# Performance work log

Hardware: AMD Instinct MI355X
Metric: run time of the kernel (lower is better)

## Reference

```python
import jax, jax.numpy as jnp
import numpy as np

D = 1024
HS = 64
NH = D // HS
NEG_INF = -1e30


def setup_inputs() -> dict:
    key = jax.random.key(0)
    ks = jax.random.split(key, 8)
    B, S = 4, 2048
    x = jax.random.normal(ks[0], (B, S, D), dtype=jnp.float32)
    y = jax.random.normal(ks[1], (B, S, D), dtype=jnp.float32)
    pad_mask = jnp.ones((B, S), dtype=jnp.int32)
    time_attention = jnp.ones((S, S), dtype=jnp.int32)
    scale = 1.0 / np.sqrt(D)
    Wq = jax.random.normal(ks[2], (D, D), dtype=jnp.float32) * scale
    Wk = jax.random.normal(ks[3], (D, D), dtype=jnp.float32) * scale
    Wv = jax.random.normal(ks[4], (D, D), dtype=jnp.float32) * scale
    Wp = jax.random.normal(ks[5], (D, D), dtype=jnp.float32) * scale
    bp = jnp.zeros((D,), dtype=jnp.float32)
    return {"x": x, "y": y, "pad_mask": pad_mask, "time_attention": time_attention,
            "Wq": Wq, "Wk": Wk, "Wv": Wv, "Wp": Wp, "bp": bp}


def reference(x, y, pad_mask, time_attention, Wq, Wk, Wv, Wp, bp):
    B, S, _ = x.shape
    Sy = y.shape[1]
    # q/k/v projections (Linear: x @ W.T), split into heads -> [B, H, S, hs]
    q = (y @ Wq.T).reshape(B, Sy, NH, HS).transpose(0, 2, 1, 3)
    k = (x @ Wk.T).reshape(B, S, NH, HS).transpose(0, 2, 1, 3)
    v = (x @ Wv.T).reshape(B, S, NH, HS).transpose(0, 2, 1, 3)
    # scaled scores [B, H, Sy, S]
    att = jnp.einsum('bhqe,bhke->bhqk', q, k) * (HS ** -0.5)
    # causal mask (tril[:S, :S])
    causal = jnp.tril(jnp.ones((S, S), dtype=jnp.bool_))
    att = jnp.where(causal[None, None, :Sy, :], att, NEG_INF)
    # pad mask over kv positions
    att = jnp.where(pad_mask[:, None, None, :] != 0, att, NEG_INF)
    # time attention mask [Sq, Sk]
    att = jnp.where(time_attention[None, None, :Sy, :] != 0, att, NEG_INF)
    p = jax.nn.softmax(att, axis=-1)  # dropout p=0 -> identity
    out = jnp.einsum('bhqk,bhke->bhqe', p, v)
    out = out.transpose(0, 2, 1, 3).reshape(B, Sy, D)
    return out @ Wp.T + bp
```

## Files before the change

### kernel.cpp

```cpp
#include <hip/hip_runtime.h>
#include <hip/hip_bf16.h>
#include <stdint.h>
#include <stddef.h>


typedef __attribute__((ext_vector_type(4))) float f32x4;
typedef __attribute__((ext_vector_type(8))) short s16x8;
typedef __attribute__((ext_vector_type(4))) float float4v;
typedef __attribute__((ext_vector_type(2))) unsigned int u32x2;

#define DEV __device__ __forceinline__

constexpr int Bsz = 4, Sseq = 2048, Dm = 1024, NHn = 16, HSn = 64;
constexpr float QSCALE = 0.125f * 1.4426950408889634f;

constexpr size_t SZ_BF_XY = (size_t)Bsz * Sseq * Dm * 2;
constexpr size_t SZ_W     = (size_t)Dm * Dm * 2;
constexpr size_t OFF_XBF  = 0;
constexpr size_t OFF_YBF  = OFF_XBF + SZ_BF_XY;
constexpr size_t OFF_WQ   = OFF_YBF + SZ_BF_XY;
constexpr size_t OFF_WK   = OFF_WQ + SZ_W;
constexpr size_t OFF_WV   = OFF_WK + SZ_W;
constexpr size_t OFF_WP   = OFF_WV + SZ_W;
constexpr size_t OFF_QWS  = OFF_WP + SZ_W;
constexpr size_t OFF_KWS  = OFF_QWS + SZ_BF_XY;
constexpr size_t OFF_VTWS = OFF_KWS + SZ_BF_XY;
constexpr size_t OFF_OWS  = OFF_VTWS + SZ_BF_XY;
constexpr size_t OFF_FLAG = OFF_OWS + SZ_BF_XY;

DEV unsigned short f2bf(float f) {
  union { float f; unsigned int u; } v; v.f = f;
  unsigned int r = (v.u + 0x7FFFu + ((v.u >> 16) & 1u)) >> 16;
  return (unsigned short)r;
}

DEV void gll16(const void* g, void* l) {
  __builtin_amdgcn_global_load_lds((const __attribute__((address_space(1))) unsigned int*)g,
                                   (__attribute__((address_space(3))) unsigned int*)l, 16, 0, 0);
}

DEV unsigned int cvtpk(float a, float b) {
  unsigned int r;
  asm("v_cvt_pk_bf16_f32 %0, %1, %2" : "=v"(r) : "v"(a), "v"(b));
  return r;
}

__global__ void cvt_all(const float* __restrict__ x, const float* __restrict__ y,
                        const float* __restrict__ Wq, const float* __restrict__ Wk,
                        const float* __restrict__ Wv, const float* __restrict__ Wp,
                        char* __restrict__ ws) {
  const int blk = blockIdx.x;
  const float* src;
  unsigned short* dst;
  int b8;
  float scale = 1.f;
  if (blk < 4096)      { src = x;  dst = (unsigned short*)(ws + OFF_XBF); b8 = blk; }
  else if (blk < 8192) { src = y;  dst = (unsigned short*)(ws + OFF_YBF); b8 = blk - 4096; }
  else if (blk < 8704) { src = Wq; dst = (unsigned short*)(ws + OFF_WQ);  b8 = blk - 8192; scale = QSCALE; }
  else if (blk < 9216) { src = Wk; dst = (unsigned short*)(ws + OFF_WK);  b8 = blk - 8704; }
  else if (blk < 9728) { src = Wv; dst = (unsigned short*)(ws + OFF_WV);  b8 = blk - 9216; }
  else                 { src = Wp; dst = (unsigned short*)(ws + OFF_WP);  b8 = blk - 9728; }
  const size_t i = (size_t)b8 * 256 + threadIdx.x;
  const float4v* s = (const float4v*)src + i * 2;
  float4v a = s[0], b = s[1];
  s16x8 o;
  o[0] = (short)f2bf(a[0] * scale); o[1] = (short)f2bf(a[1] * scale);
  o[2] = (short)f2bf(a[2] * scale); o[3] = (short)f2bf(a[3] * scale);
  o[4] = (short)f2bf(b[0] * scale); o[5] = (short)f2bf(b[1] * scale);
  o[6] = (short)f2bf(b[2] * scale); o[7] = (short)f2bf(b[3] * scale);
  *(s16x8*)(dst + i * 8) = o;
}

__global__ void init_flag(int* f) { f[0] = 1; }
__global__ void check_mask(const int* __restrict__ p, int n, int* __restrict__ f) {
  int bad = 0;
  for (int i = blockIdx.x * blockDim.x + threadIdx.x; i < n; i += gridDim.x * blockDim.x)
    bad |= (p[i] == 0);
  if (bad) atomicAnd(f, 0);
}

DEV void gemm_core(const unsigned short* __restrict__ A, const unsigned short* __restrict__ W,
                   unsigned short* __restrict__ lA, unsigned short* __restrict__ lB,
                   f32x4 (&acc)[4][4], int m0, int n0, int w, int lane, int lo, int hi,
                   int wm, int wn) {
  constexpr int K = 1024;
  for (int k0 = 0; k0 < K; k0 += 32) {
#pragma unroll
    for (int h = 0; h < 2; ++h) {
      int c = w * 64 + h * 256 + lane;
      gll16(A + (size_t)(m0 + (c >> 2)) * K + k0 + (c & 3) * 8, lA + (size_t)(w * 64 + h * 256) * 8);
      gll16(W + (size_t)(n0 + (c >> 2)) * K + k0 + (c & 3) * 8, lB + (size_t)(w * 64 + h * 256) * 8);
    }
    __syncthreads();
    s16x8 af[4], bfr[4];
#pragma unroll
    for (int mi = 0; mi < 4; ++mi) af[mi] = *(const s16x8*)&lA[(wm * 64 + mi * 16 + lo) * 32 + hi * 8];
#pragma unroll
    for (int ni = 0; ni < 4; ++ni) bfr[ni] = *(const s16x8*)&lB[(wn * 64 + ni * 16 + lo) * 32 + hi * 8];
#pragma unroll
    for (int mi = 0; mi < 4; ++mi)
#pragma unroll
      for (int ni = 0; ni < 4; ++ni)
        acc[mi][ni] = __builtin_amdgcn_mfma_f32_16x16x32_bf16(af[mi], bfr[ni], acc[mi][ni], 0, 0, 0);
    __syncthreads();
  }
}

__global__ __launch_bounds__(256) void qkv_gemm(const unsigned short* __restrict__ xbf,
                                                const unsigned short* __restrict__ ybf,
                                                const unsigned short* __restrict__ wqb,
                                                const unsigned short* __restrict__ wkb,
                                                const unsigned short* __restrict__ wvb,
                                                unsigned short* __restrict__ qws,
                                                unsigned short* __restrict__ kws,
                                                unsigned short* __restrict__ vtw) {
  __shared__ unsigned short sm[17408];
  unsigned short* lA = sm;
  unsigned short* lB = sm + 4096;
  const int tid = threadIdx.x;
  const int w = tid >> 6, lane = tid & 63, lo = lane & 15, hi = lane >> 4;
  const int wm = w >> 1, wn = w & 1;
  const int m0 = blockIdx.x * 128, n0 = blockIdx.y * 128;
  const int z = blockIdx.z;
  const unsigned short* A = (z == 0) ? ybf : xbf;
  const unsigned short* W = (z == 0) ? wqb : ((z == 1) ? wkb : wvb);
  f32x4 acc[4][4] = {};
  gemm_core(A, W, lA, lB, acc, m0, n0, w, lane, lo, hi, wm, wn);

  if (z <= 1) {
    unsigned short* outb = (z == 0) ? qws : kws;
#pragma unroll
    for (int mi = 0; mi < 4; ++mi)
#pragma unroll
      for (int ni = 0; ni < 4; ++ni)
#pragma unroll
        for (int j = 0; j < 4; ++j) {
          int m = m0 + wm * 64 + mi * 16 + hi * 4 + j;
          int n = n0 + wn * 64 + ni * 16 + lo;
          int b = m >> 11, s = m & 2047, hh = n >> 6, e = n & 63;
          outb[((size_t)(b * NHn + hh) * Sseq + s) * HSn + e] = f2bf(acc[mi][ni][j]);
        }
  } else {
    __syncthreads();
#pragma unroll
    for (int mi = 0; mi < 4; ++mi)
#pragma unroll
      for (int ni = 0; ni < 4; ++ni)
#pragma unroll
        for (int j = 0; j < 4; ++j) {
          int ml = wm * 64 + mi * 16 + hi * 4 + j;
          int nl = wn * 64 + ni * 16 + lo;
          sm[(size_t)nl * 136 + ml] = f2bf(acc[mi][ni][j]);
        }
    __syncthreads();
    int nl = tid >> 1, half = tid & 1;
    int b = m0 >> 11, hh = (n0 + nl) >> 6, e = (n0 + nl) & 63;
    unsigned short* dst = vtw + ((size_t)(b * NHn + hh) * HSn + e) * Sseq + (m0 & 2047) + half * 64;
#pragma unroll
    for (int i = 0; i < 8; ++i)
      *(s16x8*)(dst + i * 8) = *(const s16x8*)&sm[(size_t)nl * 136 + half * 64 + i * 8];
  }
}

__global__ __launch_bounds__(256) void gemm_p(const unsigned short* __restrict__ A,
                                              const unsigned short* __restrict__ W,
                                              float* __restrict__ outf,
                                              const float* __restrict__ bias) {
  __shared__ unsigned short sm[8192];
  unsigned short* lA = sm;
  unsigned short* lB = sm + 4096;
  const int tid = threadIdx.x;
  const int w = tid >> 6, lane = tid & 63, lo = lane & 15, hi = lane >> 4;
  const int wm = w >> 1, wn = w & 1;
  const int m0 = blockIdx.x * 128, n0 = blockIdx.y * 128;
  f32x4 acc[4][4] = {};
  gemm_core(A, W, lA, lB, acc, m0, n0, w, lane, lo, hi, wm, wn);
  float bv[4];
#pragma unroll
  for (int ni = 0; ni < 4; ++ni) bv[ni] = bias[n0 + wn * 64 + ni * 16 + lo];
#pragma unroll
  for (int mi = 0; mi < 4; ++mi)
#pragma unroll
    for (int ni = 0; ni < 4; ++ni)
#pragma unroll
      for (int j = 0; j < 4; ++j) {
        int m = m0 + wm * 64 + mi * 16 + hi * 4 + j;
        int n = n0 + wn * 64 + ni * 16 + lo;
        outf[(size_t)m * 1024 + n] = acc[mi][ni][j] + bv[ni];
      }
}

DEV void attn_unit16(const unsigned short* __restrict__ kbc,
                     const unsigned short* __restrict__ vbc,
                     const s16x8 (&qf)[2], f32x4 (&oacc)[4],
                     float& mrun, float& lrun,
                     unsigned short* __restrict__ pbw,
                     int k0, int qw0, int lo, int hi, int b,
                     const int* __restrict__ pad, const int* __restrict__ tmask,
                     bool trivial) {
  if (k0 > qw0 + 15) return;

  f32x4 st[4];
#pragma unroll
  for (int t = 0; t < 4; ++t) {
    f32x4 z = {0.f, 0.f, 0.f, 0.f};
#pragma unroll
    for (int kk = 0; kk < 2; ++kk) {
      s16x8 kfr = *(const s16x8*)&kbc[(t * 16 + lo) * 72 + kk * 32 + hi * 8];
      z = __builtin_amdgcn_mfma_f32_16x16x32_bf16(kfr, qf[kk], z, 0, 0, 0);
    }
    st[t] = z;
  }
  const int qg = qw0 + lo;
  if (k0 + 63 > qw0) {
#pragma unroll
    for (int t = 0; t < 4; ++t)
#pragma unroll
      for (int j = 0; j < 4; ++j)
        if (k0 + t * 16 + hi * 4 + j > qg) st[t][j] = -3e38f;
  }
  if (!trivial) {
#pragma unroll
    for (int t = 0; t < 4; ++t)
#pragma unroll
      for (int j = 0; j < 4; ++j) {
        int kg = k0 + t * 16 + hi * 4 + j;
        if (!pad[b * Sseq + kg] || !tmask[(size_t)qg * Sseq + kg]) st[t][j] = -3e38f;
      }
  }
  float m0v = fmaxf(fmaxf(st[0][0], st[0][1]), fmaxf(st[0][2], st[0][3]));
  float m1v = fmaxf(fmaxf(st[1][0], st[1][1]), fmaxf(st[1][2], st[1][3]));
  float m2v = fmaxf(fmaxf(st[2][0], st[2][1]), fmaxf(st[2][2], st[2][3]));
  float m3v = fmaxf(fmaxf(st[3][0], st[3][1]), fmaxf(st[3][2], st[3][3]));
  float mx = fmaxf(fmaxf(m0v, m1v), fmaxf(m2v, m3v));
  mx = fmaxf(mx, __shfl_xor(mx, 16, 64));
  mx = fmaxf(mx, __shfl_xor(mx, 32, 64));
  const float mnew = fmaxf(mrun, mx);
  const float al = __builtin_amdgcn_exp2f(mrun - mnew);
  mrun = mnew;
  float r0 = 0.f, r1 = 0.f, r2 = 0.f, r3 = 0.f;
#pragma unroll
  for (int j = 0; j < 4; ++j) {
    float p0 = __builtin_amdgcn_exp2f(st[0][j] - mnew); st[0][j] = p0; r0 += p0;
    float p1 = __builtin_amdgcn_exp2f(st[1][j] - mnew); st[1][j] = p1; r1 += p1;
    float p2 = __builtin_amdgcn_exp2f(st[2][j] - mnew); st[2][j] = p2; r2 += p2;
    float p3 = __builtin_amdgcn_exp2f(st[3][j] - mnew); st[3][j] = p3; r3 += p3;
  }
  float rs = (r0 + r1) + (r2 + r3);
  rs += __shfl_xor(rs, 16, 64);
  rs += __shfl_xor(rs, 32, 64);
  lrun = lrun * al + rs;
#pragma unroll
  for (int et = 0; et < 4; ++et) oacc[et] *= al;
#pragma unroll
  for (int t = 0; t < 4; ++t) {
    u32x2 dd = {cvtpk(st[t][0], st[t][1]), cvtpk(st[t][2], st[t][3])};
    *(u32x2*)&pbw[lo * 72 + t * 16 + hi * 4] = dd;
  }
  s16x8 pf[2];
#pragma unroll
  for (int kk = 0; kk < 2; ++kk)
    pf[kk] = *(const s16x8*)&pbw[lo * 72 + kk * 32 + hi * 8];
#pragma unroll
  for (int et = 0; et < 4; ++et)
#pragma unroll
    for (int kk = 0; kk < 2; ++kk) {
      s16x8 vfr = *(const s16x8*)&vbc[(et * 16 + lo) * 72 + kk * 32 + hi * 8];
      oacc[et] = __builtin_amdgcn_mfma_f32_16x16x32_bf16(vfr, pf[kk], oacc[et], 0, 0, 0);
    }
}

DEV void attn_epi16(f32x4 (&oacc)[4], float lrun,
                    unsigned short* __restrict__ pbw,
                    unsigned short* __restrict__ O, int b, int hh, int qw0,
                    int lane, int lo, int hi) {
  const float inv = 1.f / lrun;
#pragma unroll
  for (int et = 0; et < 4; ++et) {
    f32x4 o = oacc[et] * inv;
    u32x2 d = {cvtpk(o[0], o[1]), cvtpk(o[2], o[3])};
    *(u32x2*)&pbw[lo * 72 + et * 16 + hi * 4] = d;
  }
  int q = lane >> 2, seg = lane & 3;
  unsigned short* dst = O + ((size_t)b * Sseq + qw0 + q) * Dm + hh * HSn + seg * 16;
  *(s16x8*)dst = *(const s16x8*)&pbw[q * 72 + seg * 16];
  *(s16x8*)(dst + 8) = *(const s16x8*)&pbw[q * 72 + seg * 16 + 8];
}

__global__ __launch_bounds__(512, 4) void attn_kernel(const unsigned short* __restrict__ Q,
                                                      const unsigned short* __restrict__ Kg,
                                                      const unsigned short* __restrict__ Vt,
                                                      unsigned short* __restrict__ O,
                                                      const int* __restrict__ pad,
                                                      const int* __restrict__ tmask,
                                                      const int* __restrict__ flags) {
  __shared__ unsigned short kb[2][64 * 72];
  __shared__ unsigned short vb[2][64 * 72];
  __shared__ unsigned short pb[8][16 * 72];

  const int ip = blockIdx.x, bh = blockIdx.y;
  const int b = bh >> 4, hh = bh & 15;
  const int tid = threadIdx.x, w = tid >> 6, lane = tid & 63, lo = lane & 15, hi = lane >> 4;
  const int qtA = ip, qtB = 15 - ip;
  const int qw0A = qtA * 128 + w * 16, qw0B = qtB * 128 + w * 16;
  const int ktA = 2 * qtA + 1;
  const int ktmax = 2 * qtB + 2;
  const bool trivial = flags[0] != 0;

  const unsigned short* Qb = Q + (size_t)bh * Sseq * HSn;
  const unsigned short* Kb = Kg + (size_t)bh * Sseq * HSn;
  const unsigned short* Vb = Vt + (size_t)bh * HSn * Sseq;

  s16x8 qfA[2], qfB[2];
#pragma unroll
  for (int kk = 0; kk < 2; ++kk) {
    qfA[kk] = *(const s16x8*)&Qb[(size_t)(qw0A + lo) * HSn + kk * 32 + hi * 8];
    qfB[kk] = *(const s16x8*)&Qb[(size_t)(qw0B + lo) * HSn + kk * 32 + hi * 8];
  }

  f32x4 oaccA[4] = {}, oaccB[4] = {};
  float mrunA = -3e38f, lrunA = 0.f, mrunB = -3e38f, lrunB = 0.f;

  const int shalf = tid >> 8, st_t = tid & 255;
  const int sr = st_t >> 2, sc = (st_t & 3) * 16;

  s16x8 r0, r1;
  if (shalf == 0) {
    const unsigned short* gk = Kb + (size_t)sr * HSn + sc;
    r0 = *(const s16x8*)gk; r1 = *(const s16x8*)(gk + 8);
    *(s16x8*)&kb[0][sr * 72 + sc] = r0; *(s16x8*)&kb[0][sr * 72 + sc + 8] = r1;
  } else {
    const unsigned short* gv = Vb + (size_t)sr * Sseq + sc;
    r0 = *(const s16x8*)gv; r1 = *(const s16x8*)(gv + 8);
    *(s16x8*)&vb[0][sr * 72 + sc] = r0; *(s16x8*)&vb[0][sr * 72 + sc + 8] = r1;
  }
  __syncthreads();

  for (int kt = 0; kt < ktmax; ++kt) {
    const int cur = kt & 1, k0 = kt * 64;
    const bool pre = (kt + 1 < ktmax);
    if (pre) {
      const int k1 = k0 + 64;
      if (shalf == 0) {
        const unsigned short* gk = Kb + (size_t)(k1 + sr) * HSn + sc;
        r0 = *(const s16x8*)gk; r1 = *(const s16x8*)(gk + 8);
      } else {
        const unsigned short* gv = Vb + (size_t)sr * Sseq + k1 + sc;
        r0 = *(const s16x8*)gv; r1 = *(const s16x8*)(gv + 8);
      }
    }
    const unsigned short* kbc = kb[cur];
    const unsigned short* vbc = vb[cur];
    if (kt <= ktA)
      attn_unit16(kbc, vbc, qfA, oaccA, mrunA, lrunA, pb[w],
                  k0, qw0A, lo, hi, b, pad, tmask, trivial);
    attn_unit16(kbc, vbc, qfB, oaccB, mrunB, lrunB, pb[w],
                k0, qw0B, lo, hi, b, pad, tmask, trivial);
    if (pre) {
      const int nb = cur ^ 1;
      if (shalf == 0) {
        *(s16x8*)&kb[nb][sr * 72 + sc] = r0; *(s16x8*)&kb[nb][sr * 72 + sc + 8] = r1;
      } else {
        *(s16x8*)&vb[nb][sr * 72 + sc] = r0; *(s16x8*)&vb[nb][sr * 72 + sc + 8] = r1;
      }
    }
    __syncthreads();
  }

  attn_epi16(oaccA, lrunA, pb[w], O, b, hh, qw0A, lane, lo, hi);
  attn_epi16(oaccB, lrunB, pb[w], O, b, hh, qw0B, lane, lo, hi);
}

extern "C" void kernel_launch(void* const* d_in, const int* in_sizes, int n_in,
                              void* d_out, int out_size, void* d_ws, size_t ws_size,
                              hipStream_t stream) {
  const float* x = (const float*)d_in[0];
  const float* y = (const float*)d_in[1];
  const int* pad = (const int*)d_in[2];
  const int* tmask = (const int*)d_in[3];
  const float* Wq = (const float*)d_in[4];
  const float* Wk = (const float*)d_in[5];
  const float* Wv = (const float*)d_in[6];
  const float* Wp = (const float*)d_in[7];
  const float* bp = (const float*)d_in[8];

  char* ws = (char*)d_ws;
  unsigned short* xbf = (unsigned short*)(ws + OFF_XBF);
  unsigned short* ybf = (unsigned short*)(ws + OFF_YBF);
  unsigned short* wqb = (unsigned short*)(ws + OFF_WQ);
  unsigned short* wkb = (unsigned short*)(ws + OFF_WK);
  unsigned short* wvb = (unsigned short*)(ws + OFF_WV);
  unsigned short* wpb = (unsigned short*)(ws + OFF_WP);
  unsigned short* qws = (unsigned short*)(ws + OFF_QWS);
  unsigned short* kws = (unsigned short*)(ws + OFF_KWS);
  unsigned short* vtw = (unsigned short*)(ws + OFF_VTWS);
  unsigned short* ows = (unsigned short*)(ws + OFF_OWS);
  int* flags = (int*)(ws + OFF_FLAG);

  init_flag<<<1, 1, 0, stream>>>(flags);
  check_mask<<<64, 256, 0, stream>>>(pad, Bsz * Sseq, flags);
  check_mask<<<2048, 256, 0, stream>>>(tmask, Sseq * Sseq, flags);

  cvt_all<<<10240, 256, 0, stream>>>(x, y, Wq, Wk, Wv, Wp, ws);

  qkv_gemm<<<dim3(64, 8, 3), 256, 0, stream>>>(xbf, ybf, wqb, wkb, wvb, qws, kws, vtw);

  attn_kernel<<<dim3(8, 64), 512, 0, stream>>>(qws, kws, vtw, ows, pad, tmask, flags);

  gemm_p<<<dim3(64, 8), 256, 0, stream>>>(ows, wpb, (float*)d_out, bp);
}
```

Measured before the change: 206.6 us.

## Fold mask checks into conversion kernel and fuse K/V projection GEMMs

The separate flag-init and two mask-check kernels are removed. The mask scan now runs as extra blocks of the bf16 conversion kernel, using vectorized loads and one wave-level ballot plus atomicOr per wave, with the flag polarity inverted and cleared by a memset. The combined QKV GEMM is split into a Q GEMM and a fused K/V GEMM that loads each x tile once and computes both projections, which halves the A-tile traffic for K and V. In exchange, the K/V kernel holds twice the accumulators, which raises register pressure and may lower occupancy. It also adds one more kernel launch.

```diff
diff --git a/kernel.cpp b/kernel.cpp
--- a/kernel.cpp
+++ b/kernel.cpp
@@ -7,6 +7,7 @@
 typedef __attribute__((ext_vector_type(4))) float f32x4;
 typedef __attribute__((ext_vector_type(8))) short s16x8;
 typedef __attribute__((ext_vector_type(4))) float float4v;
+typedef __attribute__((ext_vector_type(4))) int i32x4;
 typedef __attribute__((ext_vector_type(2))) unsigned int u32x2;
 
 #define DEV __device__ __forceinline__
@@ -48,8 +49,24 @@
 __global__ void cvt_all(const float* __restrict__ x, const float* __restrict__ y,
                         const float* __restrict__ Wq, const float* __restrict__ Wk,
                         const float* __restrict__ Wv, const float* __restrict__ Wp,
-                        char* __restrict__ ws) {
+                        const int* __restrict__ pad, const int* __restrict__ tmask,
+                        char* __restrict__ ws, int* __restrict__ flags) {
   const int blk = blockIdx.x;
+  if (blk >= 10240) {
+    int bad = 0;
+    if (blk < 10248) {
+      const i32x4 v = ((const i32x4*)pad)[(blk - 10240) * 256 + threadIdx.x];
+      bad = (v[0] == 0) | (v[1] == 0) | (v[2] == 0) | (v[3] == 0);
+    } else {
+      const i32x4* tp = (const i32x4*)tmask + ((size_t)(blk - 10248) * 256 + threadIdx.x) * 2;
+      i32x4 v0 = tp[0], v1 = tp[1];
+      bad = (v0[0] == 0) | (v0[1] == 0) | (v0[2] == 0) | (v0[3] == 0) |
+            (v1[0] == 0) | (v1[1] == 0) | (v1[2] == 0) | (v1[3] == 0);
+    }
+    if (__builtin_amdgcn_ballot_w64(bad) != 0 && (threadIdx.x & 63) == 0)
+      atomicOr(flags, 1);
+    return;
+  }
   const float* src;
   unsigned short* dst;
   int b8;
@@ -71,101 +88,10 @@
   *(s16x8*)(dst + i * 8) = o;
 }
 
-__global__ void init_flag(int* f) { f[0] = 1; }
-__global__ void check_mask(const int* __restrict__ p, int n, int* __restrict__ f) {
-  int bad = 0;
-  for (int i = blockIdx.x * blockDim.x + threadIdx.x; i < n; i += gridDim.x * blockDim.x)
-    bad |= (p[i] == 0);
-  if (bad) atomicAnd(f, 0);
-}
-
-DEV void gemm_core(const unsigned short* __restrict__ A, const unsigned short* __restrict__ W,
-                   unsigned short* __restrict__ lA, unsigned short* __restrict__ lB,
-                   f32x4 (&acc)[4][4], int m0, int n0, int w, int lane, int lo, int hi,
-                   int wm, int wn) {
+__global__ __launch_bounds__(256) void q_gemm(const unsigned short* __restrict__ A,
+                                              const unsigned short* __restrict__ W,
+                                              unsigned short* __restrict__ outb) {
   constexpr int K = 1024;
-  for (int k0 = 0; k0 < K; k0 += 32) {
-#pragma unroll
-    for (int h = 0; h < 2; ++h) {
-      int c = w * 64 + h * 256 + lane;
-      gll16(A + (size_t)(m0 + (c >> 2)) * K + k0 + (c & 3) * 8, lA + (size_t)(w * 64 + h * 256) * 8);
-      gll16(W + (size_t)(n0 + (c >> 2)) * K + k0 + (c & 3) * 8, lB + (size_t)(w * 64 + h * 256) * 8);
-    }
-    __syncthreads();
-    s16x8 af[4], bfr[4];
-#pragma unroll
-    for (int mi = 0; mi < 4; ++mi) af[mi] = *(const s16x8*)&lA[(wm * 64 + mi * 16 + lo) * 32 + hi * 8];
-#pragma unroll
-    for (int ni = 0; ni < 4; ++ni) bfr[ni] = *(const s16x8*)&lB[(wn * 64 + ni * 16 + lo) * 32 + hi * 8];
-#pragma unroll
-    for (int mi = 0; mi < 4; ++mi)
-#pragma unroll
-      for (int ni = 0; ni < 4; ++ni)
-        acc[mi][ni] = __builtin_amdgcn_mfma_f32_16x16x32_bf16(af[mi], bfr[ni], acc[mi][ni], 0, 0, 0);
-    __syncthreads();
-  }
-}
-
-__global__ __launch_bounds__(256) void qkv_gemm(const unsigned short* __restrict__ xbf,
-                                                const unsigned short* __restrict__ ybf,
-                                                const unsigned short* __restrict__ wqb,
-                                                const unsigned short* __restrict__ wkb,
-                                                const unsigned short* __restrict__ wvb,
-                                                unsigned short* __restrict__ qws,
-                                                unsigned short* __restrict__ kws,
-                                                unsigned short* __restrict__ vtw) {
-  __shared__ unsigned short sm[17408];
-  unsigned short* lA = sm;
-  unsigned short* lB = sm + 4096;
-  const int tid = threadIdx.x;
-  const int w = tid >> 6, lane = tid & 63, lo = lane & 15, hi = lane >> 4;
-  const int wm = w >> 1, wn = w & 1;
-  const int m0 = blockIdx.x * 128, n0 = blockIdx.y * 128;
-  const int z = blockIdx.z;
-  const unsigned short* A = (z == 0) ? ybf : xbf;
-  const unsigned short* W = (z == 0) ? wqb : ((z == 1) ? wkb : wvb);
-  f32x4 acc[4][4] = {};
-  gemm_core(A, W, lA, lB, acc, m0, n0, w, lane, lo, hi, wm, wn);
-
-  if (z <= 1) {
-    unsigned short* outb = (z == 0) ? qws : kws;
-#pragma unroll
-    for (int mi = 0; mi < 4; ++mi)
-#pragma unroll
-      for (int ni = 0; ni < 4; ++ni)
-#pragma unroll
-        for (int j = 0; j < 4; ++j) {
-          int m = m0 + wm * 64 + mi * 16 + hi * 4 + j;
-          int n = n0 + wn * 64 + ni * 16 + lo;
-          int b = m >> 11, s = m & 2047, hh = n >> 6, e = n & 63;
-          outb[((size_t)(b * NHn + hh) * Sseq + s) * HSn + e] = f2bf(acc[mi][ni][j]);
-        }
-  } else {
-    __syncthreads();
-#pragma unroll
-    for (int mi = 0; mi < 4; ++mi)
-#pragma unroll
-      for (int ni = 0; ni < 4; ++ni)
-#pragma unroll
-        for (int j = 0; j < 4; ++j) {
-          int ml = wm * 64 + mi * 16 + hi * 4 + j;
-          int nl = wn * 64 + ni * 16 + lo;
-          sm[(size_t)nl * 136 + ml] = f2bf(acc[mi][ni][j]);
-        }
-    __syncthreads();
-    int nl = tid >> 1, half = tid & 1;
-    int b = m0 >> 11, hh = (n0 + nl) >> 6, e = (n0 + nl) & 63;
-    unsigned short* dst = vtw + ((size_t)(b * NHn + hh) * HSn + e) * Sseq + (m0 & 2047) + half * 64;
-#pragma unroll
-    for (int i = 0; i < 8; ++i)
-      *(s16x8*)(dst + i * 8) = *(const s16x8*)&sm[(size_t)nl * 136 + half * 64 + i * 8];
-  }
-}
-
-__global__ __launch_bounds__(256) void gemm_p(const unsigned short* __restrict__ A,
-                                              const unsigned short* __restrict__ W,
-                                              float* __restrict__ outf,
-                                              const float* __restrict__ bias) {
   __shared__ unsigned short sm[8192];
   unsigned short* lA = sm;
   unsigned short* lB = sm + 4096;
@@ -174,7 +100,149 @@
   const int wm = w >> 1, wn = w & 1;
   const int m0 = blockIdx.x * 128, n0 = blockIdx.y * 128;
   f32x4 acc[4][4] = {};
-  gemm_core(A, W, lA, lB, acc, m0, n0, w, lane, lo, hi, wm, wn);
+
+  for (int k0 = 0; k0 < K; k0 += 32) {
+#pragma unroll
+    for (int h = 0; h < 2; ++h) {
+      int c = w * 64 + h * 256 + lane;
+      gll16(A + (size_t)(m0 + (c >> 2)) * K + k0 + (c & 3) * 8, lA + (size_t)(w * 64 + h * 256) * 8);
+      gll16(W + (size_t)(n0 + (c >> 2)) * K + k0 + (c & 3) * 8, lB + (size_t)(w * 64 + h * 256) * 8);
+    }
+    __syncthreads();
+    s16x8 af[4], bfr[4];
+#pragma unroll
+    for (int mi = 0; mi < 4; ++mi) af[mi] = *(const s16x8*)&lA[(wm * 64 + mi * 16 + lo) * 32 + hi * 8];
+#pragma unroll
+    for (int ni = 0; ni < 4; ++ni) bfr[ni] = *(const s16x8*)&lB[(wn * 64 + ni * 16 + lo) * 32 + hi * 8];
+#pragma unroll
+    for (int mi = 0; mi < 4; ++mi)
+#pragma unroll
+      for (int ni = 0; ni < 4; ++ni)
+        acc[mi][ni] = __builtin_amdgcn_mfma_f32_16x16x32_bf16(af[mi], bfr[ni], acc[mi][ni], 0, 0, 0);
+    __syncthreads();
+  }
+#pragma unroll
+  for (int mi = 0; mi < 4; ++mi)
+#pragma unroll
+    for (int ni = 0; ni < 4; ++ni)
+#pragma unroll
+      for (int j = 0; j < 4; ++j) {
+        int m = m0 + wm * 64 + mi * 16 + hi * 4 + j;
+        int n = n0 + wn * 64 + ni * 16 + lo;
+        int b = m >> 11, s = m & 2047, hh = n >> 6, e = n & 63;
+        outb[((size_t)(b * NHn + hh) * Sseq + s) * HSn + e] = f2bf(acc[mi][ni][j]);
+      }
+}
+
+__global__ __launch_bounds__(256, 2) void kv_gemm(const unsigned short* __restrict__ A,
+                                                  const unsigned short* __restrict__ Wk,
+                                                  const unsigned short* __restrict__ Wv,
+                                                  unsigned short* __restrict__ kws,
+                                                  unsigned short* __restrict__ vtw) {
+  constexpr int K = 1024;
+  __shared__ unsigned short sm[17408];
+  unsigned short* lA = sm;
+  unsigned short* lBk = sm + 4096;
+  unsigned short* lBv = sm + 8192;
+  const int tid = threadIdx.x;
+  const int w = tid >> 6, lane = tid & 63, lo = lane & 15, hi = lane >> 4;
+  const int wm = w >> 1, wn = w & 1;
+  const int m0 = blockIdx.x * 128, n0 = blockIdx.y * 128;
+  f32x4 acck[4][4] = {}, accv[4][4] = {};
+
+  for (int k0 = 0; k0 < K; k0 += 32) {
+#pragma unroll
+    for (int h = 0; h < 2; ++h) {
+      int c = w * 64 + h * 256 + lane;
+      size_t roff = (size_t)(c >> 2) * K + k0 + (c & 3) * 8;
+      size_t loff = (size_t)(w * 64 + h * 256) * 8;
+      gll16(A + (size_t)m0 * K + roff, lA + loff);
+      gll16(Wk + (size_t)n0 * K + roff, lBk + loff);
+      gll16(Wv + (size_t)n0 * K + roff, lBv + loff);
+    }
+    __syncthreads();
+    s16x8 af[4], bfk[4], bfv[4];
+#pragma unroll
+    for (int mi = 0; mi < 4; ++mi) af[mi] = *(const s16x8*)&lA[(wm * 64 + mi * 16 + lo) * 32 + hi * 8];
+#pragma unroll
+    for (int ni = 0; ni < 4; ++ni) {
+      bfk[ni] = *(const s16x8*)&lBk[(wn * 64 + ni * 16 + lo) * 32 + hi * 8];
+      bfv[ni] = *(const s16x8*)&lBv[(wn * 64 + ni * 16 + lo) * 32 + hi * 8];
+    }
+#pragma unroll
+    for (int mi = 0; mi < 4; ++mi)
+#pragma unroll
+      for (int ni = 0; ni < 4; ++ni) {
+        acck[mi][ni] = __builtin_amdgcn_mfma_f32_16x16x32_bf16(af[mi], bfk[ni], acck[mi][ni], 0, 0, 0);
+        accv[mi][ni] = __builtin_amdgcn_mfma_f32_16x16x32_bf16(af[mi], bfv[ni], accv[mi][ni], 0, 0, 0);
+      }
+    __syncthreads();
+  }
+
+#pragma unroll
+  for (int mi = 0; mi < 4; ++mi)
+#pragma unroll
+    for (int ni = 0; ni < 4; ++ni)
+#pragma unroll
+      for (int j = 0; j < 4; ++j) {
+        int m = m0 + wm * 64 + mi * 16 + hi * 4 + j;
+        int n = n0 + wn * 64 + ni * 16 + lo;
+        int b = m >> 11, s = m & 2047, hh = n >> 6, e = n & 63;
+        kws[((size_t)(b * NHn + hh) * Sseq + s) * HSn + e] = f2bf(acck[mi][ni][j]);
+      }
+  __syncthreads();
+#pragma unroll
+  for (int mi = 0; mi < 4; ++mi)
+#pragma unroll
+    for (int ni = 0; ni < 4; ++ni)
+#pragma unroll
+      for (int j = 0; j < 4; ++j) {
+        int ml = wm * 64 + mi * 16 + hi * 4 + j;
+        int nl = wn * 64 + ni * 16 + lo;
+        sm[(size_t)nl * 136 + ml] = f2bf(accv[mi][ni][j]);
+      }
+  __syncthreads();
+  int nl = tid >> 1, half = tid & 1;
+  int b = m0 >> 11, hh = (n0 + nl) >> 6, e = (n0 + nl) & 63;
+  unsigned short* dst = vtw + ((size_t)(b * NHn + hh) * HSn + e) * Sseq + (m0 & 2047) + half * 64;
+#pragma unroll
+  for (int i = 0; i < 8; ++i)
+    *(s16x8*)(dst + i * 8) = *(const s16x8*)&sm[(size_t)nl * 136 + half * 64 + i * 8];
+}
+
+__global__ __launch_bounds__(256) void gemm_p(const unsigned short* __restrict__ A,
+                                              const unsigned short* __restrict__ W,
+                                              float* __restrict__ outf,
+                                              const float* __restrict__ bias) {
+  constexpr int K = 1024;
+  __shared__ unsigned short sm[8192];
+  unsigned short* lA = sm;
+  unsigned short* lB = sm + 4096;
+  const int tid = threadIdx.x;
+  const int w = tid >> 6, lane = tid & 63, lo = lane & 15, hi = lane >> 4;
+  const int wm = w >> 1, wn = w & 1;
+  const int m0 = blockIdx.x * 128, n0 = blockIdx.y * 128;
+  f32x4 acc[4][4] = {};
+  for (int k0 = 0; k0 < K; k0 += 32) {
+#pragma unroll
+    for (int h = 0; h < 2; ++h) {
+      int c = w * 64 + h * 256 + lane;
+      gll16(A + (size_t)(m0 + (c >> 2)) * K + k0 + (c & 3) * 8, lA + (size_t)(w * 64 + h * 256) * 8);
+      gll16(W + (size_t)(n0 + (c >> 2)) * K + k0 + (c & 3) * 8, lB + (size_t)(w * 64 + h * 256) * 8);
+    }
+    __syncthreads();
+    s16x8 af[4], bfr[4];
+#pragma unroll
+    for (int mi = 0; mi < 4; ++mi) af[mi] = *(const s16x8*)&lA[(wm * 64 + mi * 16 + lo) * 32 + hi * 8];
+#pragma unroll
+    for (int ni = 0; ni < 4; ++ni) bfr[ni] = *(const s16x8*)&lB[(wn * 64 + ni * 16 + lo) * 32 + hi * 8];
+#pragma unroll
+    for (int mi = 0; mi < 4; ++mi)
+#pragma unroll
+      for (int ni = 0; ni < 4; ++ni)
+        acc[mi][ni] = __builtin_amdgcn_mfma_f32_16x16x32_bf16(af[mi], bfr[ni], acc[mi][ni], 0, 0, 0);
+    __syncthreads();
+  }
   float bv[4];
 #pragma unroll
   for (int ni = 0; ni < 4; ++ni) bv[ni] = bias[n0 + wn * 64 + ni * 16 + lo];
@@ -305,7 +373,7 @@
   const int qw0A = qtA * 128 + w * 16, qw0B = qtB * 128 + w * 16;
   const int ktA = 2 * qtA + 1;
   const int ktmax = 2 * qtB + 2;
-  const bool trivial = flags[0] != 0;
+  const bool trivial = flags[0] == 0;
 
   const unsigned short* Qb = Q + (size_t)bh * Sseq * HSn;
   const unsigned short* Kb = Kg + (size_t)bh * Sseq * HSn;
@@ -397,13 +465,11 @@
   unsigned short* ows = (unsigned short*)(ws + OFF_OWS);
   int* flags = (int*)(ws + OFF_FLAG);
 
-  init_flag<<<1, 1, 0, stream>>>(flags);
-  check_mask<<<64, 256, 0, stream>>>(pad, Bsz * Sseq, flags);
-  check_mask<<<2048, 256, 0, stream>>>(tmask, Sseq * Sseq, flags);
-
-  cvt_all<<<10240, 256, 0, stream>>>(x, y, Wq, Wk, Wv, Wp, ws);
-
-  qkv_gemm<<<dim3(64, 8, 3), 256, 0, stream>>>(xbf, ybf, wqb, wkb, wvb, qws, kws, vtw);
+  hipMemsetAsync(flags, 0, 4, stream);
+  cvt_all<<<12296, 256, 0, stream>>>(x, y, Wq, Wk, Wv, Wp, pad, tmask, ws, flags);
+
+  q_gemm<<<dim3(64, 8), 256, 0, stream>>>(ybf, wqb, qws);
+  kv_gemm<<<dim3(64, 8), 256, 0, stream>>>(xbf, wkb, wvb, kws, vtw);
 
   attn_kernel<<<dim3(8, 64), 512, 0, stream>>>(qws, kws, vtw, ows, pad, tmask, flags);
 
```

Result: faster. 199.6 us (-3.4%).
